# Kernel optimization log

Measured on AMD Instinct MI355X. Metric: run time of the kernel, lower is better.

The kernel has to match this reference:

```python
import jax, jax.numpy as jnp
import numpy as np

N = 100000          # unique nodes in batch (= node_num here)
E_RAND = 1600000    # random edges (avg degree 16)
IN_DIM = 256
OUT_DIM = 128
MASK = (1.0, 1.0, 0.0, 0.0)  # self-loop weight per aggregator index


def setup_inputs() -> dict:
    key = jax.random.key(0)
    k = jax.random.split(key, 4)
    features = jax.random.normal(k[0], (N, IN_DIM), jnp.float32) * 0.1
    W1 = jax.random.normal(k[1], (IN_DIM, OUT_DIM), jnp.float32) / np.sqrt(IN_DIM)
    b1 = jnp.zeros((OUT_DIM,), jnp.float32)
    W2 = jax.random.normal(k[2], (OUT_DIM, OUT_DIM), jnp.float32) / np.sqrt(OUT_DIM)
    b2 = jnp.zeros((OUT_DIM,), jnp.float32)
    rnd_edges = jax.random.randint(k[3], (E_RAND, 2), 0, N, jnp.int32)
    self_loops = jnp.stack([jnp.arange(N, dtype=jnp.int32)] * 2, axis=1)  # exercise mask[ind]
    edges = jnp.concatenate([rnd_edges, self_loops], axis=0)  # [E,2] (src, dst)
    nodes = jnp.arange(N, dtype=jnp.int32)
    return {"features": features, "W1": W1, "b1": b1, "W2": W2, "b2": b2,
            "nodes": nodes, "edges": edges, "ind": 2}


def reference(features, W1, b1, W2, b2, nodes, edges, ind):
    # gather(unique nodes == arange(N)) + Linear-Tanh-Linear
    h = jnp.tanh(features @ W1 + b1) @ W2 + b2                 # [N, OUT_DIM]
    src, dst = edges[:, 0], edges[:, 1]
    mval = jnp.asarray(MASK, jnp.float32)[ind]                 # self-loop weight
    vals = jnp.where(src == dst, mval, jnp.float32(1.0))       # [E]
    # spmm(matrix, ones) -> per-row degree; spmm(matrix, h) -> weighted neighbor sum
    row_sum = jax.ops.segment_sum(vals, src, num_segments=N)   # [N]
    agg = jax.ops.segment_sum(vals[:, None] * h[dst], src, num_segments=N)  # [N, OUT_DIM]
    row_sum = jnp.where(row_sum == 0, jnp.float32(1.0), row_sum)
    out = agg / row_sum[:, None]
    return out[nodes]
```

## Files before the change

kernel.cpp:

```cpp
#include <hip/hip_runtime.h>
#include <hip/hip_bf16.h>

#define INDIM 256
#define OUTDIM 128
#define BUCKET_CAP 64

typedef __attribute__((ext_vector_type(4))) float f32x4;
typedef __attribute__((ext_vector_type(8))) short bf16x8;

__device__ inline ushort f2bf(float x) {
  __hip_bfloat16 h = __float2bfloat16(x);
  return *reinterpret_cast<ushort*>(&h);
}

__global__ void convert_weights_k(const float* __restrict__ W1, const float* __restrict__ W2,
                                  ushort* __restrict__ w1t, ushort* __restrict__ w2t) {
  int i = blockIdx.x * blockDim.x + threadIdx.x;
  if (i < INDIM * OUTDIM) {
    int col = i / INDIM, k = i % INDIM;
    w1t[i] = f2bf(W1[k * OUTDIM + col]);
  }
  if (i < OUTDIM * OUTDIM) {
    int col = i / OUTDIM, k = i % OUTDIM;
    w2t[i] = f2bf(W2[k * OUTDIM + col]);
  }
}

__global__ __launch_bounds__(256) void mlp1_k(const float* __restrict__ feat,
      const ushort* __restrict__ w1t, const float* __restrict__ b1,
      ushort* __restrict__ t_ws, int n) {
  __shared__ ushort As[64 * 256];
  const int tid = threadIdx.x;
  const int row0 = blockIdx.x * 64;
  #pragma unroll
  for (int s = 0; s < 16; ++s) {
    int e = s * 1024 + tid * 4;
    int r = e >> 8, c = e & 255;
    int gr = row0 + r;
    float4 f = make_float4(0.f, 0.f, 0.f, 0.f);
    if (gr < n) f = *reinterpret_cast<const float4*>(feat + (size_t)gr * INDIM + c);
    ushort4 u;
    u.x = f2bf(f.x); u.y = f2bf(f.y); u.z = f2bf(f.z); u.w = f2bf(f.w);
    int bo = (r * 512 + c * 2) ^ ((r & 7) << 4);
    *reinterpret_cast<ushort4*>(reinterpret_cast<char*>(As) + bo) = u;
  }
  __syncthreads();
  const int wave = tid >> 6, lane = tid & 63;
  const int l15 = lane & 15, lhi = lane >> 4;
  const int arow = wave * 16 + l15;
  f32x4 acc[8];
  #pragma unroll
  for (int nt = 0; nt < 8; ++nt) acc[nt] = (f32x4){0.f, 0.f, 0.f, 0.f};
  #pragma unroll
  for (int ks = 0; ks < 8; ++ks) {
    int kk = ks * 32 + lhi * 8;
    int ao = (arow * 512 + kk * 2) ^ ((arow & 7) << 4);
    bf16x8 afrag = *reinterpret_cast<bf16x8*>(reinterpret_cast<char*>(As) + ao);
    #pragma unroll
    for (int nt = 0; nt < 8; ++nt) {
      int bcol = nt * 16 + l15;
      bf16x8 bfrag = *reinterpret_cast<const bf16x8*>(w1t + bcol * INDIM + kk);
      acc[nt] = __builtin_amdgcn_mfma_f32_16x16x32_bf16(afrag, bfrag, acc[nt], 0, 0, 0);
    }
  }
  #pragma unroll
  for (int nt = 0; nt < 8; ++nt) {
    #pragma unroll
    for (int r = 0; r < 4; ++r) {
      int gr = row0 + wave * 16 + lhi * 4 + r;
      if (gr < n) {
        int col = nt * 16 + l15;
        float v = acc[nt][r] + b1[col];
        t_ws[(size_t)gr * OUTDIM + col] = f2bf(tanhf(v));
      }
    }
  }
}

__global__ __launch_bounds__(256) void mlp2_k(const ushort* __restrict__ t_ws,
      const ushort* __restrict__ w2t, const float* __restrict__ b2,
      ushort* __restrict__ h_ws, int n) {
  __shared__ ushort As[64 * 128];
  const int tid = threadIdx.x;
  const int row0 = blockIdx.x * 64;
  #pragma unroll
  for (int s = 0; s < 4; ++s) {
    int e = s * 2048 + tid * 8;
    int r = e >> 7, c = e & 127;
    int gr = row0 + r;
    bf16x8 v = (bf16x8){0, 0, 0, 0, 0, 0, 0, 0};
    if (gr < n) v = *reinterpret_cast<const bf16x8*>(t_ws + (size_t)gr * OUTDIM + c);
    int bo = (r * 256 + c * 2) ^ ((r & 7) << 4);
    *reinterpret_cast<bf16x8*>(reinterpret_cast<char*>(As) + bo) = v;
  }
  __syncthreads();
  const int wave = tid >> 6, lane = tid & 63;
  const int l15 = lane & 15, lhi = lane >> 4;
  const int arow = wave * 16 + l15;
  f32x4 acc[8];
  #pragma unroll
  for (int nt = 0; nt < 8; ++nt) acc[nt] = (f32x4){0.f, 0.f, 0.f, 0.f};
  #pragma unroll
  for (int ks = 0; ks < 4; ++ks) {
    int kk = ks * 32 + lhi * 8;
    int ao = (arow * 256 + kk * 2) ^ ((arow & 7) << 4);
    bf16x8 afrag = *reinterpret_cast<bf16x8*>(reinterpret_cast<char*>(As) + ao);
    #pragma unroll
    for (int nt = 0; nt < 8; ++nt) {
      int bcol = nt * 16 + l15;
      bf16x8 bfrag = *reinterpret_cast<const bf16x8*>(w2t + bcol * OUTDIM + kk);
      acc[nt] = __builtin_amdgcn_mfma_f32_16x16x32_bf16(afrag, bfrag, acc[nt], 0, 0, 0);
    }
  }
  #pragma unroll
  for (int nt = 0; nt < 8; ++nt) {
    #pragma unroll
    for (int r = 0; r < 4; ++r) {
      int gr = row0 + wave * 16 + lhi * 4 + r;
      if (gr < n) {
        int col = nt * 16 + l15;
        float v = acc[nt][r] + b2[col];
        h_ws[(size_t)gr * OUTDIM + col] = f2bf(v);
      }
    }
  }
}

__global__ void scatter_k(const int* __restrict__ edges, int E, int* __restrict__ cnt,
                          int* __restrict__ bucket) {
  int i = blockIdx.x * blockDim.x + threadIdx.x;
  if (i < E) {
    int2 e = reinterpret_cast<const int2*>(edges)[i];
    int p = atomicAdd(&cnt[e.x], 1);
    if (p < BUCKET_CAP) bucket[e.x * BUCKET_CAP + p] = e.y;
  }
}

__global__ __launch_bounds__(256) void aggregate_k(const ushort* __restrict__ h,
      const int* __restrict__ nodes, const int* __restrict__ cnt,
      const int* __restrict__ bucket, const int* __restrict__ indp,
      float* __restrict__ out, int nout) {
  int gtid = blockIdx.x * blockDim.x + threadIdx.x;
  int wid = gtid >> 6;
  int lane = gtid & 63;
  if (wid >= nout) return;
  int s = nodes[wid];
  int ind = indp[0] & 3;
  float mv = (ind < 2) ? 1.0f : 0.0f;
  int deg = min(cnt[s], BUCKET_CAP);
  int myd = (lane < deg) ? bucket[s * BUCKET_CAP + lane] : -1;
  float a0 = 0.f, a1 = 0.f, wsum = 0.f;
  for (int e = 0; e < deg; ++e) {
    int d = __shfl(myd, e);
    float w = (d == s) ? mv : 1.0f;
    wsum += w;
    if (w != 0.f) {
      uint u = *reinterpret_cast<const uint*>(h + (size_t)d * OUTDIM + lane * 2);
      a0 += w * __uint_as_float(u << 16);
      a1 += w * __uint_as_float(u & 0xffff0000u);
    }
  }
  float rs = (wsum == 0.f) ? 1.f : wsum;
  float2 o;
  o.x = a0 / rs;
  o.y = a1 / rs;
  *reinterpret_cast<float2*>(out + (size_t)wid * OUTDIM + lane * 2) = o;
}

extern "C" void kernel_launch(void* const* d_in, const int* in_sizes, int n_in,
                              void* d_out, int out_size, void* d_ws, size_t ws_size,
                              hipStream_t stream) {
  const float* feat  = (const float*)d_in[0];
  const float* W1    = (const float*)d_in[1];
  const float* b1    = (const float*)d_in[2];
  const float* W2    = (const float*)d_in[3];
  const float* b2    = (const float*)d_in[4];
  const int*   nodes = (const int*)d_in[5];
  const int*   edges = (const int*)d_in[6];
  const int*   indp  = (const int*)d_in[7];
  const int nnodes = in_sizes[0] / INDIM;
  const int E = in_sizes[6] / 2;
  const int nout = out_size / OUTDIM;

  char* ws = (char*)d_ws;
  size_t off = 0;
  auto alloc = [&](size_t b) { size_t r = off; off += (b + 255) & ~(size_t)255; return r; };
  ushort* w1t   = (ushort*)(ws + alloc((size_t)INDIM * OUTDIM * 2));
  ushort* w2t   = (ushort*)(ws + alloc((size_t)OUTDIM * OUTDIM * 2));
  ushort* h_ws  = (ushort*)(ws + alloc((size_t)nnodes * OUTDIM * 2));
  int*    cnt   = (int*)(ws + alloc((size_t)nnodes * 4));
  size_t shared_off = alloc((size_t)nnodes * BUCKET_CAP * 4);
  ushort* t_ws   = (ushort*)(ws + shared_off);
  int*    bucket = (int*)(ws + shared_off);

  hipMemsetAsync(cnt, 0, (size_t)nnodes * 4, stream);
  convert_weights_k<<<(INDIM * OUTDIM + 255) / 256, 256, 0, stream>>>(W1, W2, w1t, w2t);
  mlp1_k<<<(nnodes + 63) / 64, 256, 0, stream>>>(feat, w1t, b1, t_ws, nnodes);
  mlp2_k<<<(nnodes + 63) / 64, 256, 0, stream>>>(t_ws, w2t, b2, h_ws, nnodes);
  scatter_k<<<(E + 255) / 256, 256, 0, stream>>>(edges, E, cnt, bucket);
  aggregate_k<<<(nout + 3) / 4, 256, 0, stream>>>(h_ws, nodes, cnt, bucket, indp,
                                                  (float*)d_out, nout);
}
```

Baseline: 501.8 us.

## Fuse MLP layers and co-schedule edge scatter in one launch

Merges the two MLP kernels so the tanh intermediate stays in shared memory instead of going through global memory. The same launch also runs the edge bucketing, with the first blocks acting as a grid-stride scatter, so the atomic scatter can overlap the matrix work. The cnt memset is folded into the weight-prep kernel, and the aggregation loop is unrolled by two, dropping the zero-weight branch so the gathers can be issued back to back. This removes several launches and a round trip of the intermediate to global memory, but the bucket buffer no longer aliases the intermediate, so the workspace grows.

```diff
diff --git a/kernel.cpp b/kernel.cpp
--- a/kernel.cpp
+++ b/kernel.cpp
@@ -13,8 +13,9 @@
   return *reinterpret_cast<ushort*>(&h);
 }
 
-__global__ void convert_weights_k(const float* __restrict__ W1, const float* __restrict__ W2,
-                                  ushort* __restrict__ w1t, ushort* __restrict__ w2t) {
+__global__ void prep_k(const float* __restrict__ W1, const float* __restrict__ W2,
+                       ushort* __restrict__ w1t, ushort* __restrict__ w2t,
+                       int* __restrict__ cnt, int n) {
   int i = blockIdx.x * blockDim.x + threadIdx.x;
   if (i < INDIM * OUTDIM) {
     int col = i / INDIM, k = i % INDIM;
@@ -24,14 +25,28 @@
     int col = i / OUTDIM, k = i % OUTDIM;
     w2t[i] = f2bf(W2[k * OUTDIM + col]);
   }
+  if (i < n) cnt[i] = 0;
 }
 
-__global__ __launch_bounds__(256) void mlp1_k(const float* __restrict__ feat,
-      const ushort* __restrict__ w1t, const float* __restrict__ b1,
-      ushort* __restrict__ t_ws, int n) {
+__global__ __launch_bounds__(256) void fused_k(
+      const float* __restrict__ feat, const ushort* __restrict__ w1t,
+      const float* __restrict__ b1, const ushort* __restrict__ w2t,
+      const float* __restrict__ b2, ushort* __restrict__ h_ws, int n,
+      const int* __restrict__ edges, int E, int* __restrict__ cnt,
+      int* __restrict__ bucket, int nscat) {
+  const int tid = threadIdx.x;
+  const int bid = blockIdx.x;
+  if (bid < nscat) {
+    const int stride = nscat << 8;
+    for (int i = (bid << 8) + tid; i < E; i += stride) {
+      int2 e = reinterpret_cast<const int2*>(edges)[i];
+      int p = atomicAdd(&cnt[e.x], 1);
+      if (p < BUCKET_CAP) bucket[e.x * BUCKET_CAP + p] = e.y;
+    }
+    return;
+  }
   __shared__ ushort As[64 * 256];
-  const int tid = threadIdx.x;
-  const int row0 = blockIdx.x * 64;
+  const int row0 = (bid - nscat) * 64;
   #pragma unroll
   for (int s = 0; s < 16; ++s) {
     int e = s * 1024 + tid * 4;
@@ -63,43 +78,23 @@
       acc[nt] = __builtin_amdgcn_mfma_f32_16x16x32_bf16(afrag, bfrag, acc[nt], 0, 0, 0);
     }
   }
+  __syncthreads();
   #pragma unroll
   for (int nt = 0; nt < 8; ++nt) {
     #pragma unroll
     for (int r = 0; r < 4; ++r) {
-      int gr = row0 + wave * 16 + lhi * 4 + r;
-      if (gr < n) {
-        int col = nt * 16 + l15;
-        float v = acc[nt][r] + b1[col];
-        t_ws[(size_t)gr * OUTDIM + col] = f2bf(tanhf(v));
-      }
+      int row = wave * 16 + lhi * 4 + r;
+      int col = nt * 16 + l15;
+      float v = acc[nt][r] + b1[col];
+      ushort tv = f2bf(tanhf(v));
+      int bo = (row * 256 + col * 2) ^ ((row & 7) << 4);
+      *reinterpret_cast<ushort*>(reinterpret_cast<char*>(As) + bo) = tv;
     }
   }
-}
-
-__global__ __launch_bounds__(256) void mlp2_k(const ushort* __restrict__ t_ws,
-      const ushort* __restrict__ w2t, const float* __restrict__ b2,
-      ushort* __restrict__ h_ws, int n) {
-  __shared__ ushort As[64 * 128];
-  const int tid = threadIdx.x;
-  const int row0 = blockIdx.x * 64;
+  __syncthreads();
+  f32x4 acc2[8];
   #pragma unroll
-  for (int s = 0; s < 4; ++s) {
-    int e = s * 2048 + tid * 8;
-    int r = e >> 7, c = e & 127;
-    int gr = row0 + r;
-    bf16x8 v = (bf16x8){0, 0, 0, 0, 0, 0, 0, 0};
-    if (gr < n) v = *reinterpret_cast<const bf16x8*>(t_ws + (size_t)gr * OUTDIM + c);
-    int bo = (r * 256 + c * 2) ^ ((r & 7) << 4);
-    *reinterpret_cast<bf16x8*>(reinterpret_cast<char*>(As) + bo) = v;
-  }
-  __syncthreads();
-  const int wave = tid >> 6, lane = tid & 63;
-  const int l15 = lane & 15, lhi = lane >> 4;
-  const int arow = wave * 16 + l15;
-  f32x4 acc[8];
-  #pragma unroll
-  for (int nt = 0; nt < 8; ++nt) acc[nt] = (f32x4){0.f, 0.f, 0.f, 0.f};
+  for (int nt = 0; nt < 8; ++nt) acc2[nt] = (f32x4){0.f, 0.f, 0.f, 0.f};
   #pragma unroll
   for (int ks = 0; ks < 4; ++ks) {
     int kk = ks * 32 + lhi * 8;
@@ -109,7 +104,7 @@
     for (int nt = 0; nt < 8; ++nt) {
       int bcol = nt * 16 + l15;
       bf16x8 bfrag = *reinterpret_cast<const bf16x8*>(w2t + bcol * OUTDIM + kk);
-      acc[nt] = __builtin_amdgcn_mfma_f32_16x16x32_bf16(afrag, bfrag, acc[nt], 0, 0, 0);
+      acc2[nt] = __builtin_amdgcn_mfma_f32_16x16x32_bf16(afrag, bfrag, acc2[nt], 0, 0, 0);
     }
   }
   #pragma unroll
@@ -119,20 +114,10 @@
       int gr = row0 + wave * 16 + lhi * 4 + r;
       if (gr < n) {
         int col = nt * 16 + l15;
-        float v = acc[nt][r] + b2[col];
+        float v = acc2[nt][r] + b2[col];
         h_ws[(size_t)gr * OUTDIM + col] = f2bf(v);
       }
     }
-  }
-}
-
-__global__ void scatter_k(const int* __restrict__ edges, int E, int* __restrict__ cnt,
-                          int* __restrict__ bucket) {
-  int i = blockIdx.x * blockDim.x + threadIdx.x;
-  if (i < E) {
-    int2 e = reinterpret_cast<const int2*>(edges)[i];
-    int p = atomicAdd(&cnt[e.x], 1);
-    if (p < BUCKET_CAP) bucket[e.x * BUCKET_CAP + p] = e.y;
   }
 }
 
@@ -150,15 +135,25 @@
   int deg = min(cnt[s], BUCKET_CAP);
   int myd = (lane < deg) ? bucket[s * BUCKET_CAP + lane] : -1;
   float a0 = 0.f, a1 = 0.f, wsum = 0.f;
-  for (int e = 0; e < deg; ++e) {
+  int e = 0;
+  for (; e + 2 <= deg; e += 2) {
+    int d0 = __shfl(myd, e);
+    int d1 = __shfl(myd, e + 1);
+    float w0 = (d0 == s) ? mv : 1.0f;
+    float w1v = (d1 == s) ? mv : 1.0f;
+    uint u0 = *reinterpret_cast<const uint*>(h + (size_t)d0 * OUTDIM + lane * 2);
+    uint u1 = *reinterpret_cast<const uint*>(h + (size_t)d1 * OUTDIM + lane * 2);
+    wsum += w0 + w1v;
+    a0 += w0 * __uint_as_float(u0 << 16) + w1v * __uint_as_float(u1 << 16);
+    a1 += w0 * __uint_as_float(u0 & 0xffff0000u) + w1v * __uint_as_float(u1 & 0xffff0000u);
+  }
+  if (e < deg) {
     int d = __shfl(myd, e);
     float w = (d == s) ? mv : 1.0f;
+    uint u = *reinterpret_cast<const uint*>(h + (size_t)d * OUTDIM + lane * 2);
     wsum += w;
-    if (w != 0.f) {
-      uint u = *reinterpret_cast<const uint*>(h + (size_t)d * OUTDIM + lane * 2);
-      a0 += w * __uint_as_float(u << 16);
-      a1 += w * __uint_as_float(u & 0xffff0000u);
-    }
+    a0 += w * __uint_as_float(u << 16);
+    a1 += w * __uint_as_float(u & 0xffff0000u);
   }
   float rs = (wsum == 0.f) ? 1.f : wsum;
   float2 o;
@@ -185,19 +180,17 @@
   char* ws = (char*)d_ws;
   size_t off = 0;
   auto alloc = [&](size_t b) { size_t r = off; off += (b + 255) & ~(size_t)255; return r; };
-  ushort* w1t   = (ushort*)(ws + alloc((size_t)INDIM * OUTDIM * 2));
-  ushort* w2t   = (ushort*)(ws + alloc((size_t)OUTDIM * OUTDIM * 2));
-  ushort* h_ws  = (ushort*)(ws + alloc((size_t)nnodes * OUTDIM * 2));
-  int*    cnt   = (int*)(ws + alloc((size_t)nnodes * 4));
-  size_t shared_off = alloc((size_t)nnodes * BUCKET_CAP * 4);
-  ushort* t_ws   = (ushort*)(ws + shared_off);
-  int*    bucket = (int*)(ws + shared_off);
+  ushort* w1t    = (ushort*)(ws + alloc((size_t)INDIM * OUTDIM * 2));
+  ushort* w2t    = (ushort*)(ws + alloc((size_t)OUTDIM * OUTDIM * 2));
+  ushort* h_ws   = (ushort*)(ws + alloc((size_t)nnodes * OUTDIM * 2));
+  int*    cnt    = (int*)(ws + alloc((size_t)nnodes * 4));
+  int*    bucket = (int*)(ws + alloc((size_t)nnodes * BUCKET_CAP * 4));
 
-  hipMemsetAsync(cnt, 0, (size_t)nnodes * 4, stream);
-  convert_weights_k<<<(INDIM * OUTDIM + 255) / 256, 256, 0, stream>>>(W1, W2, w1t, w2t);
-  mlp1_k<<<(nnodes + 63) / 64, 256, 0, stream>>>(feat, w1t, b1, t_ws, nnodes);
-  mlp2_k<<<(nnodes + 63) / 64, 256, 0, stream>>>(t_ws, w2t, b2, h_ws, nnodes);
-  scatter_k<<<(E + 255) / 256, 256, 0, stream>>>(edges, E, cnt, bucket);
+  const int nscat = 1664;
+  const int nmlp  = (nnodes + 63) / 64;
+  prep_k<<<(nnodes + 255) / 256, 256, 0, stream>>>(W1, W2, w1t, w2t, cnt, nnodes);
+  fused_k<<<nscat + nmlp, 256, 0, stream>>>(feat, w1t, b1, w2t, b2, h_ws, nnodes,
+                                            edges, E, cnt, bucket, nscat);
   aggregate_k<<<(nout + 3) / 4, 256, 0, stream>>>(h_ws, nodes, cnt, bucket, indp,
                                                   (float*)d_out, nout);
 }
```

Measured after the change: 424.1 us. 1.18x faster.
